# Kernel tuning notes

Measured on AMD Instinct MI355X. Metric: run time of the kernel, lower is better.

## Reference

```python
import jax, jax.numpy as jnp
import numpy as np

B, A, N_IN = 128, 96, 128  # molecules, atoms per molecule, feature dim
H1, H2 = 64, 1             # gated-equivariant MLP widths: 128 -> 64 -> 1


def _mlp(x, W1, b1, W2, b2):
    return jax.nn.silu(x @ W1 + b1) @ W2 + b2


def _gated_block(s, v, Wmix, Ws1, bs1, Ws2, bs2, n_out, sact):
    # s: [N, n_sin], v: [N, 3, n_vin]
    vmix = jnp.einsum('ndi,io->ndo', v, Wmix)          # [N, 3, 2*n_out]
    vV, vW = vmix[..., :n_out], vmix[..., n_out:]
    vVn = jnp.linalg.norm(vV, axis=-2)                 # [N, n_out]
    x = _mlp(jnp.concatenate([s, vVn], axis=-1), Ws1, bs1, Ws2, bs2)
    s_out, gate = x[..., :n_out], x[..., n_out:]
    v_out = gate[:, None, :] * vW                      # [N, 3, n_out]
    if sact:
        s_out = jax.nn.silu(s_out)
    return s_out, v_out


def setup_inputs():
    key = jax.random.key(0)
    ks = iter(jax.random.split(key, 40))
    def W(shape):
        return jax.random.normal(next(ks), shape, jnp.float32) / np.sqrt(shape[0]).astype(np.float32)
    N = B * A
    return dict(
        positions=jax.random.normal(next(ks), (N, 3), jnp.float32) * 3.0,
        scalar_rep=jax.random.normal(next(ks), (N, N_IN), jnp.float32),
        vector_rep=jax.random.normal(next(ks), (N, 3, N_IN), jnp.float32),
        mix_W1=W((N_IN, 2 * H1)),
        sc1_W1=W((N_IN + H1, N_IN)), sc1_b1=jnp.zeros((N_IN,), jnp.float32),
        sc1_W2=W((N_IN, 2 * H1)), sc1_b2=jnp.zeros((2 * H1,), jnp.float32),
        mix_W2=W((H1, 2 * H2)),
        sc2_W1=W((H1 + H2, H1)), sc2_b1=jnp.zeros((H1,), jnp.float32),
        sc2_W2=W((H1, 2 * H2)), sc2_b2=jnp.zeros((2 * H2,), jnp.float32),
        vv_W1=W((9, 30)), vv_b1=jnp.zeros((30,), jnp.float32), vv_W2=W((30, 9)), vv_b2=jnp.zeros((9,), jnp.float32),
        vr_W1=W((9, 30)), vr_b1=jnp.zeros((30,), jnp.float32), vr_W2=W((30, 9)), vr_b2=jnp.zeros((9,), jnp.float32),
        s_W1=W((2, 30)), s_b1=jnp.zeros((30,), jnp.float32), s_W2=W((30, 9)), s_b2=jnp.zeros((9,), jnp.float32),
        h_W1=W((9, 30)), h_b1=jnp.zeros((30,), jnp.float32), h_W2=W((30, 9)), h_b2=jnp.zeros((9,), jnp.float32),
        n_atoms=jnp.full((B,), A, dtype=jnp.int32),
    )


def reference(positions, scalar_rep, vector_rep,
              mix_W1, sc1_W1, sc1_b1, sc1_W2, sc1_b2,
              mix_W2, sc2_W1, sc2_b1, sc2_W2, sc2_b2,
              vv_W1, vv_b1, vv_W2, vv_b2,
              vr_W1, vr_b1, vr_W2, vr_b2,
              s_W1, s_b1, s_W2, s_b2,
              h_W1, h_b1, h_W2, h_b2, n_atoms):
    # outnet: gated equivariant MLP 128 -> 64 (silu on scalars) -> 1 (no sact)
    s, v = _gated_block(scalar_rep, vector_rep, mix_W1, sc1_W1, sc1_b1, sc1_W2, sc1_b2, H1, True)
    s, v = _gated_block(s, v, mix_W2, sc2_W1, sc2_b1, sc2_W2, sc2_b2, H2, False)
    l0 = s[:, 0].reshape(B, A)          # [B, A]
    l1 = v[:, :, 0].reshape(B, A, 3)    # [B, A, 3]
    pos = positions.reshape(B, A, 3)
    # per-pair outer products, flattened 3x3 -> 9 (row-major k,l as in torch view)
    vv = jnp.einsum('bik,bjl->bijkl', l1, l1).reshape(B, A, A, 9)
    vr = jnp.einsum('bik,bjl->bijkl', l1, pos).reshape(B, A, A, 9)
    vv = _mlp(vv, vv_W1, vv_b1, vv_W2, vv_b2)
    vr = _mlp(vr, vr_W1, vr_b1, vr_W2, vr_b2)
    sp = jnp.stack([jnp.broadcast_to(l0[:, :, None], (B, A, A)),
                    jnp.broadcast_to(l0[:, None, :], (B, A, A))], axis=-1)  # [B,A,A,2] = (s_i, s_j)
    sp = _mlp(sp, s_W1, s_b1, s_W2, s_b2)
    h = _mlp(vv + vr + sp, h_W1, h_b1, h_W2, h_b2).reshape(B, A, A, 3, 3)
    # permute(0,2,1,3) per molecule -> block Hessian [3A, 3A]
    h = jnp.transpose(h, (0, 1, 3, 2, 4)).reshape(B, 3 * A, 3 * A)
    return h.reshape(-1, 27)
```

## Files before the change

### kernel.cpp

```cpp
#include <hip/hip_runtime.h>
#include <cstddef>

#define A_ATOMS 96
#define BATCH   128
#define NNODES  12288
#define NB      8
#define AS      132
#define XS      196

typedef float v2f __attribute__((ext_vector_type(2)));

__device__ __forceinline__ float silu_f(float x) {
    float e = __expf(-x);
    return x * __builtin_amdgcn_rcpf(1.0f + e);
}
__device__ __forceinline__ v2f silu2(v2f x) {
    v2f r; r.x = silu_f(x.x); r.y = silu_f(x.y); return r;
}

#define RED64(v) { v += __shfl_xor(v, 1); v += __shfl_xor(v, 2); v += __shfl_xor(v, 4); \
                   v += __shfl_xor(v, 8); v += __shfl_xor(v, 16); v += __shfl_xor(v, 32); }
#define RED16(v) { v += __shfl_xor(v, 1); v += __shfl_xor(v, 2); v += __shfl_xor(v, 4); \
                   v += __shfl_xor(v, 8); }

__global__ __launch_bounds__(128, 3)
void node_k(const float* __restrict__ vrep, const float* __restrict__ mixW1,
            const float* __restrict__ srep,
            const float* __restrict__ sc1W1, const float* __restrict__ sc1b1,
            const float* __restrict__ sc1W2, const float* __restrict__ sc1b2,
            const float* __restrict__ mixW2,
            const float* __restrict__ sc2W1, const float* __restrict__ sc2b1,
            const float* __restrict__ sc2W2, const float* __restrict__ sc2b2,
            float* __restrict__ l0v, float* __restrict__ l1v) {
    __shared__ float AsL[24 * AS];
    __shared__ float xinS[NB * XS];
    __shared__ float s1s[2][4][64];
    __shared__ float pwp[NB][6];

    const int t  = threadIdx.x;
    const int w  = t >> 6;
    const int ln = t & 63;
    const int cx = ln & 15;
    const int ry = ln >> 4;
    const int cb = w * 64 + cx * 4;
    const int row0  = blockIdx.x * 24;
    const int node0 = blockIdx.x * NB;

#pragma unroll
    for (int it = 0; it < 6; it++) {
        const int idx = it * 128 + t;
        const int r   = idx >> 5;
        const int c4  = (idx & 31) * 4;
        *(float4*)&AsL[r * AS + c4] = *(const float4*)(vrep + (size_t)(row0 + r) * 128 + c4);
    }
#pragma unroll
    for (int it = 0; it < 2; it++) {
        const int idx = it * 128 + t;
        const int a   = idx >> 5;
        const int c4  = (idx & 31) * 4;
        *(float4*)&xinS[a * XS + c4] = *(const float4*)(srep + (size_t)(node0 + a) * 128 + c4);
    }
    __syncthreads();

    float acc[2][3][4];
#pragma unroll
    for (int p = 0; p < 2; p++)
#pragma unroll
        for (int d = 0; d < 3; d++)
#pragma unroll
            for (int j = 0; j < 4; j++) acc[p][d][j] = 0.0f;

    for (int kc = 0; kc < 128; kc += 8) {
        float a[2][3][8];
#pragma unroll
        for (int p = 0; p < 2; p++)
#pragma unroll
            for (int d = 0; d < 3; d++) {
                const int row = (3 * (ry + 4 * p) + d) * AS + kc;
                *(float4*)&a[p][d][0] = *(const float4*)&AsL[row];
                *(float4*)&a[p][d][4] = *(const float4*)&AsL[row + 4];
            }
#pragma unroll
        for (int kk = 0; kk < 8; kk++) {
            float b[4];
            *(float4*)b = *(const float4*)(mixW1 + (size_t)(kc + kk) * 128 + cb);
#pragma unroll
            for (int p = 0; p < 2; p++)
#pragma unroll
                for (int d = 0; d < 3; d++)
#pragma unroll
                    for (int j = 0; j < 4; j++)
                        acc[p][d][j] += a[p][d][kk] * b[j];
        }
    }
    if (w == 0) {
#pragma unroll
        for (int p = 0; p < 2; p++) {
            float nrm[4];
#pragma unroll
            for (int c = 0; c < 4; c++)
                nrm[c] = sqrtf(acc[p][0][c] * acc[p][0][c] + acc[p][1][c] * acc[p][1][c]
                             + acc[p][2][c] * acc[p][2][c]);
            *(float4*)&xinS[(ry + 4 * p) * XS + 128 + cb] = *(float4*)nrm;
        }
    }
    __syncthreads();

    float* workS = AsL;
    {
        float acc3[2][4];
#pragma unroll
        for (int p = 0; p < 2; p++)
#pragma unroll
            for (int j = 0; j < 4; j++) acc3[p][j] = 0.0f;
        for (int kc = 0; kc < 192; kc += 8) {
            float af[2][8];
#pragma unroll
            for (int p = 0; p < 2; p++) {
                const int row = (ry + 4 * p) * XS + kc;
                *(float4*)&af[p][0] = *(const float4*)&xinS[row];
                *(float4*)&af[p][4] = *(const float4*)&xinS[row + 4];
            }
#pragma unroll
            for (int kk = 0; kk < 8; kk++) {
                float b[4];
                *(float4*)b = *(const float4*)(sc1W1 + (size_t)(kc + kk) * 128 + cb);
#pragma unroll
                for (int p = 0; p < 2; p++)
#pragma unroll
                    for (int j = 0; j < 4; j++) acc3[p][j] += af[p][kk] * b[j];
            }
        }
#pragma unroll
        for (int p = 0; p < 2; p++) {
            float h[4];
#pragma unroll
            for (int j = 0; j < 4; j++) h[j] = silu_f(acc3[p][j] + sc1b1[cb + j]);
            *(float4*)&workS[(ry + 4 * p) * AS + cb] = *(float4*)h;
        }
    }
    __syncthreads();

    float xg[2][4];
    {
        float acc4[2][4];
#pragma unroll
        for (int p = 0; p < 2; p++)
#pragma unroll
            for (int j = 0; j < 4; j++) acc4[p][j] = 0.0f;
        for (int kc = 0; kc < 128; kc += 8) {
            float af[2][8];
#pragma unroll
            for (int p = 0; p < 2; p++) {
                const int row = (ry + 4 * p) * AS + kc;
                *(float4*)&af[p][0] = *(const float4*)&workS[row];
                *(float4*)&af[p][4] = *(const float4*)&workS[row + 4];
            }
#pragma unroll
            for (int kk = 0; kk < 8; kk++) {
                float b[4];
                *(float4*)b = *(const float4*)(sc1W2 + (size_t)(kc + kk) * 128 + cb);
#pragma unroll
                for (int p = 0; p < 2; p++)
#pragma unroll
                    for (int j = 0; j < 4; j++) acc4[p][j] += af[p][kk] * b[j];
            }
        }
        if (w == 0) {
#pragma unroll
            for (int p = 0; p < 2; p++) {
                float xs[4];
#pragma unroll
                for (int j = 0; j < 4; j++) xs[j] = acc4[p][j] + sc1b2[cb + j];
                *(float4*)&xinS[(ry + 4 * p) * XS + cb] = *(float4*)xs;
            }
        } else {
#pragma unroll
            for (int p = 0; p < 2; p++)
#pragma unroll
                for (int j = 0; j < 4; j++) xg[p][j] = acc4[p][j] + sc1b2[cb + j];
        }
    }

    if (w == 1) {
#pragma unroll
        for (int p = 0; p < 2; p++) {
            float p0 = 0, p1 = 0, p2 = 0, p3 = 0, p4 = 0, p5 = 0;
#pragma unroll
            for (int c = 0; c < 4; c++) {
                float2 m = *(const float2*)(mixW2 + (size_t)(cb - 64 + c) * 2);
                const float v0 = xg[p][c] * acc[p][0][c];
                const float v1 = xg[p][c] * acc[p][1][c];
                const float v2 = xg[p][c] * acc[p][2][c];
                p0 += v0 * m.x; p1 += v0 * m.y;
                p2 += v1 * m.x; p3 += v1 * m.y;
                p4 += v2 * m.x; p5 += v2 * m.y;
            }
            RED16(p0); RED16(p1); RED16(p2); RED16(p3); RED16(p4); RED16(p5);
            if (cx == 0) {
                const int nl = ry + 4 * p;
                pwp[nl][0] = p0; pwp[nl][1] = p1;
                pwp[nl][2] = p2; pwp[nl][3] = p3;
                pwp[nl][4] = p4; pwp[nl][5] = p5;
            }
        }
    }
    __syncthreads();

    {
        const float bb1 = sc2b1[ln];
        const float wn  = sc2W1[64 * 64 + ln];
        const float wq0 = sc2W2[ln * 2 + 0], wq1 = sc2W2[ln * 2 + 1];
        float vn2[4], g0[4], g1[4], g2[4];
#pragma unroll
        for (int r = 0; r < 4; r++) {
            const int nl = r * 2 + w;
            const float q00 = pwp[nl][0], q10 = pwp[nl][2], q20 = pwp[nl][4];
            vn2[r] = sqrtf(q00 * q00 + q10 * q10 + q20 * q20);
            g0[r] = pwp[nl][1]; g1[r] = pwp[nl][3]; g2[r] = pwp[nl][5];
            s1s[w][r][ln] = silu_f(xinS[nl * XS + ln]);
        }
        __builtin_amdgcn_s_waitcnt(0);
        float acc5[4];
#pragma unroll
        for (int r = 0; r < 4; r++) acc5[r] = bb1 + vn2[r] * wn;
#pragma unroll 8
        for (int i2 = 0; i2 < 64; i2++) {
            const float wv = sc2W1[i2 * 64 + ln];
#pragma unroll
            for (int r = 0; r < 4; r++) acc5[r] += s1s[w][r][i2] * wv;
        }
#pragma unroll
        for (int r = 0; r < 4; r++) {
            const float h2 = silu_f(acc5[r]);
            float q0 = h2 * wq0, q1 = h2 * wq1;
            RED64(q0); RED64(q1);
            if (ln == 0) {
                const int n = node0 + r * 2 + w;
                const float gate = q1 + sc2b2[1];
                l0v[n] = q0 + sc2b2[0];
                l1v[(size_t)n * 3 + 0] = gate * g0[r];
                l1v[(size_t)n * 3 + 1] = gate * g1[r];
                l1v[(size_t)n * 3 + 2] = gate * g2[r];
            }
        }
    }
}

__global__ __launch_bounds__(256)
void pairpre_k(const float* __restrict__ l1v, const float* __restrict__ pos,
               const float* __restrict__ l0v,
               const float* __restrict__ vvW1, const float* __restrict__ vrW1,
               const float* __restrict__ sW1, const float* __restrict__ sb1,
               float* __restrict__ Pv, float* __restrict__ Pr,
               float* __restrict__ Ps) {
    const int jl = threadIdx.x & 31;
    const int hq = threadIdx.x >> 5;
    const int j  = blockIdx.x * 32 + jl;
    const float lj0 = l1v[j * 3 + 0], lj1 = l1v[j * 3 + 1], lj2 = l1v[j * 3 + 2];
    const float pj0 = pos[j * 3 + 0], pj1 = pos[j * 3 + 1], pj2 = pos[j * 3 + 2];
    const float l0j = l0v[j];
#pragma unroll
    for (int hh = 0; hh < 4; hh++) {
        const int h = hq * 4 + hh;
        if (h < 30) {
#pragma unroll
            for (int a = 0; a < 3; a++) {
                float v = lj0 * vvW1[(3 * a + 0) * 30 + h] + lj1 * vvW1[(3 * a + 1) * 30 + h]
                        + lj2 * vvW1[(3 * a + 2) * 30 + h];
                float r = pj0 * vrW1[(3 * a + 0) * 30 + h] + pj1 * vrW1[(3 * a + 1) * 30 + h]
                        + pj2 * vrW1[(3 * a + 2) * 30 + h];
                Pv[(size_t)(a * 30 + h) * NNODES + j] = v;
                Pr[(size_t)(a * 30 + h) * NNODES + j] = r;
            }
            Ps[(size_t)h * NNODES + j] = sb1[h] + l0j * sW1[30 + h];
        }
    }
}

__global__ __launch_bounds__(192)
void pair_k(const float* __restrict__ l0v, const float* __restrict__ l1v,
            const float* __restrict__ Pv, const float* __restrict__ Pr,
            const float* __restrict__ Ps,
            const float* __restrict__ vvb1, const float* __restrict__ vrb1,
            const float* __restrict__ sW1,
            const float* __restrict__ vvW2, const float* __restrict__ vrW2,
            const float* __restrict__ sW2,
            const float* __restrict__ vvb2, const float* __restrict__ vrb2,
            const float* __restrict__ sb2,
            const float* __restrict__ hW1,  const float* __restrict__ hb1,
            const float* __restrict__ hW2,  const float* __restrict__ hb2,
            float* __restrict__ out) {
    const int t = threadIdx.x;
    const int b = blockIdx.y;
    const int g = (t >= 96) ? 1 : 0;
    const int j = t - g * 96;
    const int i0 = blockIdx.x * 8 + g * 4;
    const int ni0 = b * A_ATOMS + i0;
    const int ni2 = ni0 + 2;
    const int nj  = b * A_ATOMS + j;

    const v2f liA0 = { l1v[ni0 * 3 + 0], l1v[(ni0 + 1) * 3 + 0] };
    const v2f liA1 = { l1v[ni0 * 3 + 1], l1v[(ni0 + 1) * 3 + 1] };
    const v2f liA2 = { l1v[ni0 * 3 + 2], l1v[(ni0 + 1) * 3 + 2] };
    const v2f s0iA = { l0v[ni0], l0v[ni0 + 1] };
    const v2f liB0 = { l1v[ni2 * 3 + 0], l1v[(ni2 + 1) * 3 + 0] };
    const v2f liB1 = { l1v[ni2 * 3 + 1], l1v[(ni2 + 1) * 3 + 1] };
    const v2f liB2 = { l1v[ni2 * 3 + 2], l1v[(ni2 + 1) * 3 + 2] };
    const v2f s0iB = { l0v[ni2], l0v[ni2 + 1] };

    v2f tA[9], tB[9];
#pragma unroll
    for (int l = 0; l < 9; l++) {
        const float t0 = vvb2[l] + vrb2[l] + sb2[l];
        tA[l] = (v2f)t0; tB[l] = (v2f)t0;
    }

#pragma unroll 2
    for (int h = 0; h < 30; h++) {
        const float pv0 = Pv[(size_t)h * NNODES + nj];
        const float pv1 = Pv[(size_t)(30 + h) * NNODES + nj];
        const float pv2 = Pv[(size_t)(60 + h) * NNODES + nj];
        const float pr0 = Pr[(size_t)h * NNODES + nj];
        const float pr1 = Pr[(size_t)(30 + h) * NNODES + nj];
        const float pr2 = Pr[(size_t)(60 + h) * NNODES + nj];
        const float ps  = Ps[(size_t)h * NNODES + nj];
        const float sw  = sW1[h];
        const float bv = vvb1[h], br = vrb1[h];

        v2f avA = (v2f)(bv) + liA0 * pv0 + liA1 * pv1 + liA2 * pv2;
        v2f arA = (v2f)(br) + liA0 * pr0 + liA1 * pr1 + liA2 * pr2;
        v2f asA = (v2f)(ps) + s0iA * sw;
        v2f avB = (v2f)(bv) + liB0 * pv0 + liB1 * pv1 + liB2 * pv2;
        v2f arB = (v2f)(br) + liB0 * pr0 + liB1 * pr1 + liB2 * pr2;
        v2f asB = (v2f)(ps) + s0iB * sw;
        avA = silu2(avA); arA = silu2(arA); asA = silu2(asA);
        avB = silu2(avB); arB = silu2(arB); asB = silu2(asB);
#pragma unroll
        for (int l = 0; l < 9; l++) {
            const float w2v = vvW2[h * 9 + l];
            const float w2r = vrW2[h * 9 + l];
            const float w2s = sW2[h * 9 + l];
            tA[l] += avA * w2v + arA * w2r + asA * w2s;
            tB[l] += avB * w2v + arB * w2r + asB * w2s;
        }
    }

    v2f oA[9], oB[9];
#pragma unroll
    for (int l = 0; l < 9; l++) {
        oA[l] = (v2f)(hb2[l]); oB[l] = (v2f)(hb2[l]);
    }
#pragma unroll 2
    for (int h = 0; h < 30; h++) {
        v2f aA = (v2f)(hb1[h]), aB = (v2f)(hb1[h]);
#pragma unroll
        for (int m = 0; m < 9; m++) {
            const float w1 = hW1[m * 30 + h];
            aA += tA[m] * w1; aB += tB[m] * w1;
        }
        aA = silu2(aA); aB = silu2(aB);
#pragma unroll
        for (int l = 0; l < 9; l++) {
            const float w2 = hW2[h * 9 + l];
            oA[l] += aA * w2; oB[l] += aB * w2;
        }
    }

#pragma unroll
    for (int k = 0; k < 3; k++) {
        const size_t offA0 = ((size_t)ni0 * 3 + k) * 288 + (size_t)j * 3;
        const size_t offA1 = offA0 + 3 * 288;
        out[offA0 + 0] = oA[3 * k + 0].x;
        out[offA0 + 1] = oA[3 * k + 1].x;
        out[offA0 + 2] = oA[3 * k + 2].x;
        out[offA1 + 0] = oA[3 * k + 0].y;
        out[offA1 + 1] = oA[3 * k + 1].y;
        out[offA1 + 2] = oA[3 * k + 2].y;
        const size_t offB0 = ((size_t)ni2 * 3 + k) * 288 + (size_t)j * 3;
        const size_t offB1 = offB0 + 3 * 288;
        out[offB0 + 0] = oB[3 * k + 0].x;
        out[offB0 + 1] = oB[3 * k + 1].x;
        out[offB0 + 2] = oB[3 * k + 2].x;
        out[offB1 + 0] = oB[3 * k + 0].y;
        out[offB1 + 1] = oB[3 * k + 1].y;
        out[offB1 + 2] = oB[3 * k + 2].y;
    }
}

extern "C" void kernel_launch(void* const* d_in, const int* in_sizes, int n_in,
                              void* d_out, int out_size, void* d_ws, size_t ws_size,
                              hipStream_t stream) {
    const float* pos   = (const float*)d_in[0];
    const float* srep  = (const float*)d_in[1];
    const float* vrep  = (const float*)d_in[2];
    const float* mixW1 = (const float*)d_in[3];
    const float* sc1W1 = (const float*)d_in[4];
    const float* sc1b1 = (const float*)d_in[5];
    const float* sc1W2 = (const float*)d_in[6];
    const float* sc1b2 = (const float*)d_in[7];
    const float* mixW2 = (const float*)d_in[8];
    const float* sc2W1 = (const float*)d_in[9];
    const float* sc2b1 = (const float*)d_in[10];
    const float* sc2W2 = (const float*)d_in[11];
    const float* sc2b2 = (const float*)d_in[12];
    const float* vvW1  = (const float*)d_in[13];
    const float* vvb1  = (const float*)d_in[14];
    const float* vvW2  = (const float*)d_in[15];
    const float* vvb2  = (const float*)d_in[16];
    const float* vrW1  = (const float*)d_in[17];
    const float* vrb1  = (const float*)d_in[18];
    const float* vrW2  = (const float*)d_in[19];
    const float* vrb2  = (const float*)d_in[20];
    const float* sW1   = (const float*)d_in[21];
    const float* sb1   = (const float*)d_in[22];
    const float* sW2   = (const float*)d_in[23];
    const float* sb2   = (const float*)d_in[24];
    const float* hW1   = (const float*)d_in[25];
    const float* hb1   = (const float*)d_in[26];
    const float* hW2   = (const float*)d_in[27];
    const float* hb2   = (const float*)d_in[28];

    float* ws  = (float*)d_ws;
    float* Pv  = ws;
    float* Pr  = Pv + 1105920;
    float* Ps  = Pr + 1105920;
    float* l0v = Ps + 368640;
    float* l1v = l0v + 12288;
    float* outf = (float*)d_out;

    node_k<<<NNODES / NB, 128, 0, stream>>>(
        vrep, mixW1, srep,
        sc1W1, sc1b1, sc1W2, sc1b2,
        mixW2, sc2W1, sc2b1, sc2W2, sc2b2,
        l0v, l1v);

    pairpre_k<<<NNODES / 32, 256, 0, stream>>>(l1v, pos, l0v, vvW1, vrW1,
                                               sW1, sb1, Pv, Pr, Ps);

    pair_k<<<dim3(A_ATOMS / 8, BATCH), 192, 0, stream>>>(
        l0v, l1v, Pv, Pr, Ps,
        vvb1, vrb1, sW1,
        vvW2, vrW2, sW2,
        vvb2, vrb2, sb2,
        hW1, hb1, hW2, hb2,
        outf);
}
```

Measured before the change: 262.7 us.

## Fuse pair-precompute into node kernel and double-buffer weight loads in GEMMs

Removes the separate pairpre kernel launch by computing the per-node first-layer projections (Pv, Pr, Ps) at the end of node_k from shared-memory gate and l0 values, writing into one contiguous P buffer. It also restructures the three dense matmul loops to prefetch the next 8 weight rows into registers (wA/wB ping-pong) while computing the current chunk, to hide global load latency. This saves a launch and a reread of l0v/l1v, but adds register pressure under launch_bounds(128,3) and makes node_k's tail write 210 strided rows per block with narrow 8-node coalescing.

```diff
diff --git a/kernel.cpp b/kernel.cpp
--- a/kernel.cpp
+++ b/kernel.cpp
@@ -31,11 +31,16 @@
             const float* __restrict__ mixW2,
             const float* __restrict__ sc2W1, const float* __restrict__ sc2b1,
             const float* __restrict__ sc2W2, const float* __restrict__ sc2b2,
-            float* __restrict__ l0v, float* __restrict__ l1v) {
+            const float* __restrict__ pos,
+            const float* __restrict__ vvW1, const float* __restrict__ vrW1,
+            const float* __restrict__ sW1,  const float* __restrict__ sb1,
+            float* __restrict__ l0v, float* __restrict__ l1v,
+            float* __restrict__ P) {
     __shared__ float AsL[24 * AS];
     __shared__ float xinS[NB * XS];
     __shared__ float s1s[2][4][64];
     __shared__ float pwp[NB][6];
+    __shared__ float gateS[NB], l0S[NB];
 
     const int t  = threadIdx.x;
     const int w  = t >> 6;
@@ -70,27 +75,38 @@
 #pragma unroll
             for (int j = 0; j < 4; j++) acc[p][d][j] = 0.0f;
 
-    for (int kc = 0; kc < 128; kc += 8) {
-        float a[2][3][8];
-#pragma unroll
-        for (int p = 0; p < 2; p++)
-#pragma unroll
-            for (int d = 0; d < 3; d++) {
-                const int row = (3 * (ry + 4 * p) + d) * AS + kc;
-                *(float4*)&a[p][d][0] = *(const float4*)&AsL[row];
-                *(float4*)&a[p][d][4] = *(const float4*)&AsL[row + 4];
-            }
-#pragma unroll
-        for (int kk = 0; kk < 8; kk++) {
-            float b[4];
-            *(float4*)b = *(const float4*)(mixW1 + (size_t)(kc + kk) * 128 + cb);
-#pragma unroll
-            for (int p = 0; p < 2; p++)
-#pragma unroll
-                for (int d = 0; d < 3; d++)
-#pragma unroll
-                    for (int j = 0; j < 4; j++)
-                        acc[p][d][j] += a[p][d][kk] * b[j];
+#define LOADW8(dst, Wmat, kc0)                                                \
+    _Pragma("unroll")                                                         \
+    for (int kk = 0; kk < 8; kk++)                                            \
+        dst[kk] = *(const float4*)((Wmat) + (size_t)((kc0) + kk) * 128 + cb);
+
+#define MIX1_HALF(wbuf, kc0)                                                  \
+    _Pragma("unroll")                                                         \
+    for (int p = 0; p < 2; p++) {                                             \
+        float a_[3][8];                                                       \
+        _Pragma("unroll")                                                     \
+        for (int d = 0; d < 3; d++) {                                         \
+            const int rr = (3 * (ry + 4 * p) + d) * AS + (kc0);               \
+            *(float4*)&a_[d][0] = *(const float4*)&AsL[rr];                   \
+            *(float4*)&a_[d][4] = *(const float4*)&AsL[rr + 4];               \
+        }                                                                     \
+        _Pragma("unroll")                                                     \
+        for (int kk = 0; kk < 8; kk++)                                        \
+            _Pragma("unroll")                                                 \
+            for (int d = 0; d < 3; d++)                                       \
+                _Pragma("unroll")                                             \
+                for (int j = 0; j < 4; j++)                                   \
+                    acc[p][d][j] += a_[d][kk] * (&wbuf[kk].x)[j];             \
+    }
+
+    {
+        float4 wA[8], wB[8];
+        LOADW8(wA, mixW1, 0);
+        for (int kc = 0; kc < 128; kc += 16) {
+            LOADW8(wB, mixW1, kc + 8);
+            MIX1_HALF(wA, kc);
+            if (kc + 16 < 128) { LOADW8(wA, mixW1, kc + 16); }
+            MIX1_HALF(wB, kc + 8);
         }
     }
     if (w == 0) {
@@ -113,23 +129,28 @@
         for (int p = 0; p < 2; p++)
 #pragma unroll
             for (int j = 0; j < 4; j++) acc3[p][j] = 0.0f;
-        for (int kc = 0; kc < 192; kc += 8) {
-            float af[2][8];
-#pragma unroll
-            for (int p = 0; p < 2; p++) {
-                const int row = (ry + 4 * p) * XS + kc;
-                *(float4*)&af[p][0] = *(const float4*)&xinS[row];
-                *(float4*)&af[p][4] = *(const float4*)&xinS[row + 4];
-            }
-#pragma unroll
-            for (int kk = 0; kk < 8; kk++) {
-                float b[4];
-                *(float4*)b = *(const float4*)(sc1W1 + (size_t)(kc + kk) * 128 + cb);
-#pragma unroll
-                for (int p = 0; p < 2; p++)
-#pragma unroll
-                    for (int j = 0; j < 4; j++) acc3[p][j] += af[p][kk] * b[j];
-            }
+
+#define SC1_HALF(accv, Sbuf, SST, wbuf, kc0)                                  \
+    _Pragma("unroll")                                                         \
+    for (int p = 0; p < 2; p++) {                                             \
+        float af[8];                                                          \
+        const int rr = (ry + 4 * p) * (SST) + (kc0);                          \
+        *(float4*)&af[0] = *(const float4*)&Sbuf[rr];                         \
+        *(float4*)&af[4] = *(const float4*)&Sbuf[rr + 4];                     \
+        _Pragma("unroll")                                                     \
+        for (int kk = 0; kk < 8; kk++)                                        \
+            _Pragma("unroll")                                                 \
+            for (int j = 0; j < 4; j++)                                       \
+                accv[p][j] += af[kk] * (&wbuf[kk].x)[j];                      \
+    }
+
+        float4 wA[8], wB[8];
+        LOADW8(wA, sc1W1, 0);
+        for (int kc = 0; kc < 192; kc += 16) {
+            LOADW8(wB, sc1W1, kc + 8);
+            SC1_HALF(acc3, xinS, XS, wA, kc);
+            if (kc + 16 < 192) { LOADW8(wA, sc1W1, kc + 16); }
+            SC1_HALF(acc3, xinS, XS, wB, kc + 8);
         }
 #pragma unroll
         for (int p = 0; p < 2; p++) {
@@ -148,23 +169,14 @@
         for (int p = 0; p < 2; p++)
 #pragma unroll
             for (int j = 0; j < 4; j++) acc4[p][j] = 0.0f;
-        for (int kc = 0; kc < 128; kc += 8) {
-            float af[2][8];
-#pragma unroll
-            for (int p = 0; p < 2; p++) {
-                const int row = (ry + 4 * p) * AS + kc;
-                *(float4*)&af[p][0] = *(const float4*)&workS[row];
-                *(float4*)&af[p][4] = *(const float4*)&workS[row + 4];
-            }
-#pragma unroll
-            for (int kk = 0; kk < 8; kk++) {
-                float b[4];
-                *(float4*)b = *(const float4*)(sc1W2 + (size_t)(kc + kk) * 128 + cb);
-#pragma unroll
-                for (int p = 0; p < 2; p++)
-#pragma unroll
-                    for (int j = 0; j < 4; j++) acc4[p][j] += af[p][kk] * b[j];
-            }
+
+        float4 wA[8], wB[8];
+        LOADW8(wA, sc1W2, 0);
+        for (int kc = 0; kc < 128; kc += 16) {
+            LOADW8(wB, sc1W2, kc + 8);
+            SC1_HALF(acc4, workS, AS, wA, kc);
+            if (kc + 16 < 128) { LOADW8(wA, sc1W2, kc + 16); }
+            SC1_HALF(acc4, workS, AS, wB, kc + 8);
         }
         if (w == 0) {
 #pragma unroll
@@ -236,44 +248,51 @@
             float q0 = h2 * wq0, q1 = h2 * wq1;
             RED64(q0); RED64(q1);
             if (ln == 0) {
-                const int n = node0 + r * 2 + w;
+                const int nl = r * 2 + w;
+                const int n = node0 + nl;
                 const float gate = q1 + sc2b2[1];
-                l0v[n] = q0 + sc2b2[0];
+                const float l0o  = q0 + sc2b2[0];
+                l0v[n] = l0o;
                 l1v[(size_t)n * 3 + 0] = gate * g0[r];
                 l1v[(size_t)n * 3 + 1] = gate * g1[r];
                 l1v[(size_t)n * 3 + 2] = gate * g2[r];
+                gateS[nl] = gate;
+                l0S[nl]   = l0o;
             }
         }
     }
-}
-
-__global__ __launch_bounds__(256)
-void pairpre_k(const float* __restrict__ l1v, const float* __restrict__ pos,
-               const float* __restrict__ l0v,
-               const float* __restrict__ vvW1, const float* __restrict__ vrW1,
-               const float* __restrict__ sW1, const float* __restrict__ sb1,
-               float* __restrict__ Pv, float* __restrict__ Pr,
-               float* __restrict__ Ps) {
-    const int jl = threadIdx.x & 31;
-    const int hq = threadIdx.x >> 5;
-    const int j  = blockIdx.x * 32 + jl;
-    const float lj0 = l1v[j * 3 + 0], lj1 = l1v[j * 3 + 1], lj2 = l1v[j * 3 + 2];
-    const float pj0 = pos[j * 3 + 0], pj1 = pos[j * 3 + 1], pj2 = pos[j * 3 + 2];
-    const float l0j = l0v[j];
-#pragma unroll
-    for (int hh = 0; hh < 4; hh++) {
-        const int h = hq * 4 + hh;
-        if (h < 30) {
-#pragma unroll
-            for (int a = 0; a < 3; a++) {
-                float v = lj0 * vvW1[(3 * a + 0) * 30 + h] + lj1 * vvW1[(3 * a + 1) * 30 + h]
+    __syncthreads();
+
+    {
+        const int nl = t & 7;
+        const int n  = node0 + nl;
+        const float lj0 = gateS[nl] * pwp[nl][1];
+        const float lj1 = gateS[nl] * pwp[nl][3];
+        const float lj2 = gateS[nl] * pwp[nl][5];
+        const float l0j = l0S[nl];
+        const float pj0 = pos[n * 3 + 0], pj1 = pos[n * 3 + 1], pj2 = pos[n * 3 + 2];
+#pragma unroll
+        for (int it = 0; it < 14; it++) {
+            const int row = (t >> 3) + it * 16;
+            if (row < 210) {
+                float val;
+                if (row < 90) {
+                    const int a = row / 30, h = row - a * 30;
+                    val = lj0 * vvW1[(3 * a + 0) * 30 + h]
+                        + lj1 * vvW1[(3 * a + 1) * 30 + h]
                         + lj2 * vvW1[(3 * a + 2) * 30 + h];
-                float r = pj0 * vrW1[(3 * a + 0) * 30 + h] + pj1 * vrW1[(3 * a + 1) * 30 + h]
+                } else if (row < 180) {
+                    const int rr = row - 90;
+                    const int a = rr / 30, h = rr - a * 30;
+                    val = pj0 * vrW1[(3 * a + 0) * 30 + h]
+                        + pj1 * vrW1[(3 * a + 1) * 30 + h]
                         + pj2 * vrW1[(3 * a + 2) * 30 + h];
-                Pv[(size_t)(a * 30 + h) * NNODES + j] = v;
-                Pr[(size_t)(a * 30 + h) * NNODES + j] = r;
+                } else {
+                    const int h = row - 180;
+                    val = sb1[h] + l0j * sW1[30 + h];
+                }
+                P[(size_t)row * NNODES + n] = val;
             }
-            Ps[(size_t)h * NNODES + j] = sb1[h] + l0j * sW1[30 + h];
         }
     }
 }
@@ -422,21 +441,20 @@
     const float* hb2   = (const float*)d_in[28];
 
     float* ws  = (float*)d_ws;
-    float* Pv  = ws;
-    float* Pr  = Pv + 1105920;
-    float* Ps  = Pr + 1105920;
-    float* l0v = Ps + 368640;
-    float* l1v = l0v + 12288;
+    float* P   = ws;
+    float* Pv  = P;
+    float* Pr  = P + (size_t)90  * NNODES;
+    float* Ps  = P + (size_t)180 * NNODES;
+    float* l0v = P + (size_t)210 * NNODES;
+    float* l1v = l0v + NNODES;
     float* outf = (float*)d_out;
 
     node_k<<<NNODES / NB, 128, 0, stream>>>(
         vrep, mixW1, srep,
         sc1W1, sc1b1, sc1W2, sc1b2,
         mixW2, sc2W1, sc2b1, sc2W2, sc2b2,
-        l0v, l1v);
-
-    pairpre_k<<<NNODES / 32, 256, 0, stream>>>(l1v, pos, l0v, vvW1, vrW1,
-                                               sW1, sb1, Pv, Pr, Ps);
+        pos, vvW1, vrW1, sW1, sb1,
+        l0v, l1v, P);
 
     pair_k<<<dim3(A_ATOMS / 8, BATCH), 192, 0, stream>>>(
         l0v, l1v, Pv, Pr, Ps,
```

Result: slower. 270.2 us (+2.9%).

## Fuse pair precompute into node kernel and store P in node-major interleaved layout

Applied to the files above, without the earlier changes.

Removes the separate pairpre kernel by computing the per-node first-layer projections at the end of node_k, reading gate/l0 from shared memory. The Pv/Pr/Ps planes are merged into one node-major buffer with 8 floats per hidden unit, so pair_k loads two float4s per h instead of seven scalar loads. This trades lane-coalesced loads for per-thread contiguous but lane-strided accesses and adds padding, relying on cache reuse across the h loop.

```diff
diff --git a/kernel.cpp b/kernel.cpp
--- a/kernel.cpp
+++ b/kernel.cpp
@@ -7,6 +7,7 @@
 #define NB      8
 #define AS      132
 #define XS      196
+#define PSTR    240
 
 typedef float v2f __attribute__((ext_vector_type(2)));
 
@@ -31,11 +32,16 @@
             const float* __restrict__ mixW2,
             const float* __restrict__ sc2W1, const float* __restrict__ sc2b1,
             const float* __restrict__ sc2W2, const float* __restrict__ sc2b2,
-            float* __restrict__ l0v, float* __restrict__ l1v) {
+            const float* __restrict__ pos,
+            const float* __restrict__ vvW1, const float* __restrict__ vrW1,
+            const float* __restrict__ sW1,  const float* __restrict__ sb1,
+            float* __restrict__ l0v, float* __restrict__ l1v,
+            float* __restrict__ P) {
     __shared__ float AsL[24 * AS];
     __shared__ float xinS[NB * XS];
     __shared__ float s1s[2][4][64];
     __shared__ float pwp[NB][6];
+    __shared__ float gateS[NB], l0S[NB];
 
     const int t  = threadIdx.x;
     const int w  = t >> 6;
@@ -236,52 +242,53 @@
             float q0 = h2 * wq0, q1 = h2 * wq1;
             RED64(q0); RED64(q1);
             if (ln == 0) {
-                const int n = node0 + r * 2 + w;
+                const int nl = r * 2 + w;
+                const int n = node0 + nl;
                 const float gate = q1 + sc2b2[1];
-                l0v[n] = q0 + sc2b2[0];
+                const float l0o  = q0 + sc2b2[0];
+                l0v[n] = l0o;
                 l1v[(size_t)n * 3 + 0] = gate * g0[r];
                 l1v[(size_t)n * 3 + 1] = gate * g1[r];
                 l1v[(size_t)n * 3 + 2] = gate * g2[r];
-            }
-        }
-    }
-}
-
-__global__ __launch_bounds__(256)
-void pairpre_k(const float* __restrict__ l1v, const float* __restrict__ pos,
-               const float* __restrict__ l0v,
-               const float* __restrict__ vvW1, const float* __restrict__ vrW1,
-               const float* __restrict__ sW1, const float* __restrict__ sb1,
-               float* __restrict__ Pv, float* __restrict__ Pr,
-               float* __restrict__ Ps) {
-    const int jl = threadIdx.x & 31;
-    const int hq = threadIdx.x >> 5;
-    const int j  = blockIdx.x * 32 + jl;
-    const float lj0 = l1v[j * 3 + 0], lj1 = l1v[j * 3 + 1], lj2 = l1v[j * 3 + 2];
-    const float pj0 = pos[j * 3 + 0], pj1 = pos[j * 3 + 1], pj2 = pos[j * 3 + 2];
-    const float l0j = l0v[j];
-#pragma unroll
-    for (int hh = 0; hh < 4; hh++) {
-        const int h = hq * 4 + hh;
-        if (h < 30) {
+                gateS[nl] = gate;
+                l0S[nl]   = l0o;
+            }
+        }
+    }
+    __syncthreads();
+
+    {
+        const int nl = t >> 4;
+        const int q  = t & 15;
+        const int n  = node0 + nl;
+        const float lj0 = gateS[nl] * pwp[nl][1];
+        const float lj1 = gateS[nl] * pwp[nl][3];
+        const float lj2 = gateS[nl] * pwp[nl][5];
+        const float l0j = l0S[nl];
+        const float pj0 = pos[n * 3 + 0], pj1 = pos[n * 3 + 1], pj2 = pos[n * 3 + 2];
+        float* Pj = P + (size_t)n * PSTR;
+        for (int h = q; h < 30; h += 16) {
+            float o[8];
 #pragma unroll
             for (int a = 0; a < 3; a++) {
-                float v = lj0 * vvW1[(3 * a + 0) * 30 + h] + lj1 * vvW1[(3 * a + 1) * 30 + h]
-                        + lj2 * vvW1[(3 * a + 2) * 30 + h];
-                float r = pj0 * vrW1[(3 * a + 0) * 30 + h] + pj1 * vrW1[(3 * a + 1) * 30 + h]
-                        + pj2 * vrW1[(3 * a + 2) * 30 + h];
-                Pv[(size_t)(a * 30 + h) * NNODES + j] = v;
-                Pr[(size_t)(a * 30 + h) * NNODES + j] = r;
-            }
-            Ps[(size_t)h * NNODES + j] = sb1[h] + l0j * sW1[30 + h];
+                o[a]     = lj0 * vvW1[(3 * a + 0) * 30 + h]
+                         + lj1 * vvW1[(3 * a + 1) * 30 + h]
+                         + lj2 * vvW1[(3 * a + 2) * 30 + h];
+                o[3 + a] = pj0 * vrW1[(3 * a + 0) * 30 + h]
+                         + pj1 * vrW1[(3 * a + 1) * 30 + h]
+                         + pj2 * vrW1[(3 * a + 2) * 30 + h];
+            }
+            o[6] = sb1[h] + l0j * sW1[30 + h];
+            o[7] = 0.0f;
+            *(float4*)&Pj[h * 8 + 0] = *(float4*)&o[0];
+            *(float4*)&Pj[h * 8 + 4] = *(float4*)&o[4];
         }
     }
 }
 
 __global__ __launch_bounds__(192)
 void pair_k(const float* __restrict__ l0v, const float* __restrict__ l1v,
-            const float* __restrict__ Pv, const float* __restrict__ Pr,
-            const float* __restrict__ Ps,
+            const float* __restrict__ P,
             const float* __restrict__ vvb1, const float* __restrict__ vrb1,
             const float* __restrict__ sW1,
             const float* __restrict__ vvW2, const float* __restrict__ vrW2,
@@ -299,6 +306,7 @@
     const int ni0 = b * A_ATOMS + i0;
     const int ni2 = ni0 + 2;
     const int nj  = b * A_ATOMS + j;
+    const float* Pj = P + (size_t)nj * PSTR;
 
     const v2f liA0 = { l1v[ni0 * 3 + 0], l1v[(ni0 + 1) * 3 + 0] };
     const v2f liA1 = { l1v[ni0 * 3 + 1], l1v[(ni0 + 1) * 3 + 1] };
@@ -318,13 +326,11 @@
 
 #pragma unroll 2
     for (int h = 0; h < 30; h++) {
-        const float pv0 = Pv[(size_t)h * NNODES + nj];
-        const float pv1 = Pv[(size_t)(30 + h) * NNODES + nj];
-        const float pv2 = Pv[(size_t)(60 + h) * NNODES + nj];
-        const float pr0 = Pr[(size_t)h * NNODES + nj];
-        const float pr1 = Pr[(size_t)(30 + h) * NNODES + nj];
-        const float pr2 = Pr[(size_t)(60 + h) * NNODES + nj];
-        const float ps  = Ps[(size_t)h * NNODES + nj];
+        const float4 w0 = *(const float4*)&Pj[h * 8 + 0];
+        const float4 w1 = *(const float4*)&Pj[h * 8 + 4];
+        const float pv0 = w0.x, pv1 = w0.y, pv2 = w0.z;
+        const float pr0 = w0.w, pr1 = w1.x, pr2 = w1.y;
+        const float ps  = w1.z;
         const float sw  = sW1[h];
         const float bv = vvb1[h], br = vrb1[h];
 
@@ -422,24 +428,20 @@
     const float* hb2   = (const float*)d_in[28];
 
     float* ws  = (float*)d_ws;
-    float* Pv  = ws;
-    float* Pr  = Pv + 1105920;
-    float* Ps  = Pr + 1105920;
-    float* l0v = Ps + 368640;
-    float* l1v = l0v + 12288;
+    float* P   = ws;
+    float* l0v = P + (size_t)PSTR * NNODES;
+    float* l1v = l0v + NNODES;
     float* outf = (float*)d_out;
 
     node_k<<<NNODES / NB, 128, 0, stream>>>(
         vrep, mixW1, srep,
         sc1W1, sc1b1, sc1W2, sc1b2,
         mixW2, sc2W1, sc2b1, sc2W2, sc2b2,
-        l0v, l1v);
-
-    pairpre_k<<<NNODES / 32, 256, 0, stream>>>(l1v, pos, l0v, vvW1, vrW1,
-                                               sW1, sb1, Pv, Pr, Ps);
+        pos, vvW1, vrW1, sW1, sb1,
+        l0v, l1v, P);
 
     pair_k<<<dim3(A_ATOMS / 8, BATCH), 192, 0, stream>>>(
-        l0v, l1v, Pv, Pr, Ps,
+        l0v, l1v, P,
         vvb1, vrb1, sW1,
         vvW2, vrW2, sW2,
         vvb2, vrb2, sb2,
```

Result: no change. 261.8 us (-0.3%).
